# Kernel optimization log

Hardware: AMD Instinct MI355X
Metric: run time of the kernel (lower is better)

Reference implementation:

```python
import jax, jax.numpy as jnp
import numpy as np

E = 1024
H = 16
CH = E // H

def setup_inputs() -> dict:
    key = jax.random.key(0)
    ks = jax.random.split(key, 9)
    s = E ** -0.5
    return {
        'x': jax.random.normal(ks[0], (4, 2048, E), dtype=jnp.float32),
        'Wq': jax.random.normal(ks[1], (E, E), dtype=jnp.float32) * s,
        'bq': jnp.zeros((E,), dtype=jnp.float32),
        'Wk': jax.random.normal(ks[2], (E, E), dtype=jnp.float32) * s,
        'bk': jnp.zeros((E,), dtype=jnp.float32),
        'Wv': jax.random.normal(ks[3], (E, E), dtype=jnp.float32) * s,
        'bv': jnp.zeros((E,), dtype=jnp.float32),
        'Wo': jax.random.normal(ks[4], (E, E), dtype=jnp.float32) * s,
        'bo': jnp.zeros((E,), dtype=jnp.float32),
    }

def _split_heads(t):
    # [..., n, H*ch] -> [..., H, n, ch]
    b, n, e = t.shape
    return t.reshape(b, n, H, CH).transpose(0, 2, 1, 3)

def reference(x, Wq, bq, Wk, bk, Wv, bv, Wo, bo):
    scale = CH ** -0.5
    q = _split_heads(x @ Wq.T + bq)  # [b,H,n,ch]
    k = _split_heads(x @ Wk.T + bk)
    v = _split_heads(x @ Wv.T + bv)
    att = jnp.einsum('bhqc,bhkc->bhqk', q, k) * scale
    att = jax.nn.softmax(att, axis=-1)
    out = jnp.einsum('bhqk,bhkc->bhqc', att, v)  # [b,H,n,ch]
    b, h, n, c = out.shape
    out = out.transpose(0, 2, 1, 3).reshape(b, n, h * c)
    return out @ Wo.T + bo
```

## Files before the change

### kernel.cpp

```cpp
#include <hip/hip_runtime.h>
#include <stdint.h>

#define EMB   1024
#define NHEAD 16
#define CHD   64
#define NB    4
#define SEQ   2048
#define NTOK  (NB * SEQ)
#define KDIM  1024

typedef __attribute__((ext_vector_type(8))) short  bf16x8;
typedef __attribute__((ext_vector_type(4))) short  short4v;
typedef __attribute__((ext_vector_type(4))) float  f32x4;
typedef __attribute__((ext_vector_type(4))) float  float4v;

__device__ __forceinline__ short f2bf(float f) {
    unsigned int u = __float_as_uint(f);
    u += 0x7fffu + ((u >> 16) & 1u);
    return (short)(u >> 16);
}

__device__ __forceinline__ void async16(const short* g, short* l) {
    __builtin_amdgcn_global_load_lds((__attribute__((address_space(1))) void const*)g,
                                     (__attribute__((address_space(3))) void*)l, 16, 0, 0);
}

__global__ __launch_bounds__(256) void cvt_all(const float* __restrict__ x,
                                               const float* __restrict__ Wq,
                                               const float* __restrict__ Wk,
                                               const float* __restrict__ Wv,
                                               const float* __restrict__ Wo,
                                               short* __restrict__ xb,
                                               short* __restrict__ Wqb,
                                               short* __restrict__ Wkb,
                                               short* __restrict__ Wvb,
                                               short* __restrict__ Wob) {
    int bid = blockIdx.x;
    const float* src;
    short* dst;
    int idx;
    if (bid < 8192) {
        src = x; dst = xb; idx = bid * 256 + threadIdx.x;
    } else {
        int w  = (bid - 8192) >> 10;
        int lb = (bid - 8192) & 1023;
        src = (w == 0) ? Wq : (w == 1) ? Wk : (w == 2) ? Wv : Wo;
        dst = (w == 0) ? Wqb : (w == 1) ? Wkb : (w == 2) ? Wvb : Wob;
        idx = lb * 256 + threadIdx.x;
    }
    float4v v = ((const float4v*)src)[idx];
    short4v s;
    s.x = f2bf(v.x); s.y = f2bf(v.y); s.z = f2bf(v.z); s.w = f2bf(v.w);
    ((short4v*)dst)[idx] = s;
}

__device__ __forceinline__ void gemm_core(const short* __restrict__ Atile,
                                          const short* __restrict__ Btile,
                                          short* As, short* Bs, f32x4 acc[4][4]) {
    const int tid  = threadIdx.x;
    const int wave = tid >> 6, lane = tid & 63;
    const int quad = lane >> 4, l16 = lane & 15;
    const int wm = (wave >> 1) * 64, wn = (wave & 1) * 64;
    const int srow = lane >> 2;
    const int scol = (lane & 3) * 8;

    for (int k0 = 0; k0 < KDIM; k0 += 32) {
        __syncthreads();
#pragma unroll
        for (int c = 0; c < 2; ++c) {
            int chunk = wave * 2 + c;
            int row = chunk * 16 + srow;
            async16(Atile + (size_t)row * KDIM + k0 + scol, As + chunk * 512);
            async16(Btile + (size_t)row * KDIM + k0 + scol, Bs + chunk * 512);
        }
        __syncthreads();
        bf16x8 af[4], bfr[4];
#pragma unroll
        for (int i = 0; i < 4; ++i)
            af[i] = *(const bf16x8*)&As[(wm + i * 16 + l16) * 32 + quad * 8];
#pragma unroll
        for (int j = 0; j < 4; ++j)
            bfr[j] = *(const bf16x8*)&Bs[(wn + j * 16 + l16) * 32 + quad * 8];
#pragma unroll
        for (int i = 0; i < 4; ++i)
#pragma unroll
            for (int j = 0; j < 4; ++j)
                acc[i][j] = __builtin_amdgcn_mfma_f32_16x16x32_bf16(af[i], bfr[j], acc[i][j], 0, 0, 0);
    }
}

#define QSCALE 0.1803368801111204f


#define MFMA16(A,B,C) __builtin_amdgcn_mfma_f32_16x16x32_bf16(A,B,C,0,0,0)
#define BARR  { __builtin_amdgcn_s_barrier(); __builtin_amdgcn_sched_barrier(0); }
#define VMC4  asm volatile("s_waitcnt vmcnt(4)" ::: "memory");
#define VMC0  asm volatile("s_waitcnt vmcnt(0)" ::: "memory");
#define PRIO1 __builtin_amdgcn_s_setprio(1);
#define PRIO0 __builtin_amdgcn_s_setprio(0);

#define STAGE_A_(BUF,H,T) { \
    async16(aS0 + (size_t)(H)*131072 + (T)*64, sm + (BUF)*32768 + (H)*8192 + stA); \
    async16(aS1 + (size_t)(H)*131072 + (T)*64, sm + (BUF)*32768 + (H)*8192 + 4096 + stA); }
#define STAGE_B_(BUF,H,T) { \
    async16(bS0 + (size_t)(H)*131072 + (T)*64, sm + (BUF)*32768 + 16384 + (H)*8192 + stA); \
    async16(bS1 + (size_t)(H)*131072 + (T)*64, sm + (BUF)*32768 + 16384 + (H)*8192 + 4096 + stA); }

#define LDB_(BUF) { \
    const short* _pb = sm + (BUF)*32768 + bro; \
    bfr[0][0] = *(const bf16x8*)(_pb + ac0);        bfr[0][1] = *(const bf16x8*)(_pb + ac1); \
    bfr[1][0] = *(const bf16x8*)(_pb + 1024 + ac0); bfr[1][1] = *(const bf16x8*)(_pb + 1024 + ac1); \
    bfr[2][0] = *(const bf16x8*)(_pb + 2048 + ac0); bfr[2][1] = *(const bf16x8*)(_pb + 2048 + ac1); \
    bfr[3][0] = *(const bf16x8*)(_pb + 3072 + ac0); bfr[3][1] = *(const bf16x8*)(_pb + 3072 + ac1); }

#define LDA_(BUF,Q) { \
    const short* _pa = sm + (BUF)*32768 + aro + (Q)*2048; \
    af[0][0] = *(const bf16x8*)(_pa + ac0);        af[0][1] = *(const bf16x8*)(_pa + ac1); \
    af[1][0] = *(const bf16x8*)(_pa + 1024 + ac0); af[1][1] = *(const bf16x8*)(_pa + 1024 + ac1); }

#define MF_(Q) { \
    acc[2*(Q)][0]   = MFMA16(af[0][0], bfr[0][0], acc[2*(Q)][0]); \
    acc[2*(Q)][0]   = MFMA16(af[0][1], bfr[0][1], acc[2*(Q)][0]); \
    acc[2*(Q)][1]   = MFMA16(af[0][0], bfr[1][0], acc[2*(Q)][1]); \
    acc[2*(Q)][1]   = MFMA16(af[0][1], bfr[1][1], acc[2*(Q)][1]); \
    acc[2*(Q)][2]   = MFMA16(af[0][0], bfr[2][0], acc[2*(Q)][2]); \
    acc[2*(Q)][2]   = MFMA16(af[0][1], bfr[2][1], acc[2*(Q)][2]); \
    acc[2*(Q)][3]   = MFMA16(af[0][0], bfr[3][0], acc[2*(Q)][3]); \
    acc[2*(Q)][3]   = MFMA16(af[0][1], bfr[3][1], acc[2*(Q)][3]); \
    acc[2*(Q)+1][0] = MFMA16(af[1][0], bfr[0][0], acc[2*(Q)+1][0]); \
    acc[2*(Q)+1][0] = MFMA16(af[1][1], bfr[0][1], acc[2*(Q)+1][0]); \
    acc[2*(Q)+1][1] = MFMA16(af[1][0], bfr[1][0], acc[2*(Q)+1][1]); \
    acc[2*(Q)+1][1] = MFMA16(af[1][1], bfr[1][1], acc[2*(Q)+1][1]); \
    acc[2*(Q)+1][2] = MFMA16(af[1][0], bfr[2][0], acc[2*(Q)+1][2]); \
    acc[2*(Q)+1][2] = MFMA16(af[1][1], bfr[2][1], acc[2*(Q)+1][2]); \
    acc[2*(Q)+1][3] = MFMA16(af[1][0], bfr[3][0], acc[2*(Q)+1][3]); \
    acc[2*(Q)+1][3] = MFMA16(af[1][1], bfr[3][1], acc[2*(Q)+1][3]); }

#define WINDOW(RB, AB, TA, BB, TB) \
    LDB_(RB) LDA_(RB,0) STAGE_A_(AB,0,TA) BARR \
    PRIO1 MF_(0) PRIO0 BARR \
    LDA_(RB,1) STAGE_A_(AB,1,TA) BARR \
    PRIO1 MF_(1) PRIO0 BARR \
    LDA_(RB,2) STAGE_B_(BB,0,TB) BARR \
    PRIO1 MF_(2) PRIO0 BARR \
    LDA_(RB,3) STAGE_B_(BB,1,TB) BARR \
    PRIO1 MF_(3) PRIO0 VMC4 BARR

__global__ __launch_bounds__(512, 2) void qk256(const short* __restrict__ xb,
                                                const short* __restrict__ Wqk,
                                                const float* __restrict__ bq,
                                                const float* __restrict__ bk,
                                                short* __restrict__ Qb,
                                                short* __restrict__ Kb) {
    extern __shared__ short sm[];
    const int bm = blockIdx.x, bn = blockIdx.y;
    const int tid = threadIdx.x;
    const int w = tid >> 6, lane = tid & 63;
    const int kq = lane >> 4, l16 = lane & 15;
    const int wmi = w >> 2, wni = w & 3;

    const int colsw = ((lane & 7) * 8) ^ (((lane >> 5) & 1) << 4);
    const short* aS0 = xb  + (size_t)(bm * 256 + w * 8 + (lane >> 3)) * 1024 + colsw;
    const short* aS1 = aS0 + (size_t)64 * 1024;
    const short* bS0 = Wqk + (size_t)(bn * 256 + w * 8 + (lane >> 3)) * 1024 + colsw;
    const short* bS1 = bS0 + (size_t)64 * 1024;
    const int stA = w * 512;

    const int swz = (l16 & 4) ? 16 : 0;
    const int ac0 = (kq * 8) ^ swz;
    const int ac1 = (32 + kq * 8) ^ swz;
    const int aro = wmi * 8192 + l16 * 64;
    const int bro = 16384 + (wni >> 1) * 8192 + ((wni & 1) * 64 + l16) * 64;

    f32x4 acc[8][4];
    const f32x4 z = {0.f, 0.f, 0.f, 0.f};
#pragma unroll
    for (int m = 0; m < 8; ++m)
#pragma unroll
        for (int n = 0; n < 4; ++n) acc[m][n] = z;
    bf16x8 bfr[4][2], af[2][2];

    STAGE_A_(0,0,0) STAGE_A_(0,1,0) STAGE_B_(0,0,0) STAGE_B_(0,1,0)
    STAGE_B_(1,0,1) STAGE_B_(1,1,1)
    VMC4 BARR

    for (int it = 0; it < 7; ++it) {
        const int te = 2 * it;
        WINDOW(0, 1, te + 1, 0, te + 2)
        WINDOW(1, 0, te + 2, 1, te + 3)
    }
    LDB_(0) LDA_(0,0) STAGE_A_(1,0,15) BARR
    PRIO1 MF_(0) PRIO0 BARR
    LDA_(0,1) STAGE_A_(1,1,15) BARR
    PRIO1 MF_(1) PRIO0 BARR
    LDA_(0,2) BARR
    PRIO1 MF_(2) PRIO0 BARR
    LDA_(0,3) BARR
    PRIO1 MF_(3) PRIO0 VMC0 BARR
    LDB_(1)
    LDA_(1,0) MF_(0)
    LDA_(1,1) MF_(1)
    LDA_(1,2) MF_(2)
    LDA_(1,3) MF_(3)

    const bool isQ = (bn < 4);
    const float* bias = isQ ? bq : bk;
    short* dst = isQ ? Qb : Kb;
    const float sc = isQ ? QSCALE : 1.0f;
    const int fb = (bn & 3) * 256 + wni * 64 + l16;
    const int tok0 = bm * 256 + wmi * 128 + kq * 4;
#pragma unroll
    for (int n = 0; n < 4; ++n) {
        const int e = fb + n * 16;
        const int hh = e >> 6, cc = e & 63;
        const float bv_ = bias[e];
#pragma unroll
        for (int m = 0; m < 8; ++m)
#pragma unroll
            for (int r = 0; r < 4; ++r) {
                const int tok = tok0 + m * 16 + r;
                const int bb = tok >> 11, nn = tok & 2047;
                dst[(((size_t)bb * NHEAD + hh) * SEQ + nn) * CHD + cc] =
                    f2bf((acc[m][n][r] + bv_) * sc);
            }
    }
}

__global__ __launch_bounds__(256) void vproj(const short* __restrict__ xb,
                                             const short* __restrict__ Wvb,
                                             const float* __restrict__ bv,
                                             short* __restrict__ Vtb) {
    __shared__ short As[128 * 32], Bs[128 * 32];
    const int bm = blockIdx.x;
    const int ew = blockIdx.y * 128;

    f32x4 acc[4][4];
    const f32x4 z = {0.f, 0.f, 0.f, 0.f};
#pragma unroll
    for (int i = 0; i < 4; ++i)
#pragma unroll
        for (int j = 0; j < 4; ++j) acc[i][j] = z;

    gemm_core(Wvb + (size_t)ew * KDIM, xb + (size_t)bm * 128 * KDIM, As, Bs, acc);

    const int lane = threadIdx.x & 63, wave = threadIdx.x >> 6;
    const int quad = lane >> 4, l16 = lane & 15;
    const int wm = (wave >> 1) * 64, wn = (wave & 1) * 64;
#pragma unroll
    for (int i = 0; i < 4; ++i)
#pragma unroll
        for (int j = 0; j < 4; ++j)
#pragma unroll
            for (int r = 0; r < 4; ++r) {
                int e = ew + wm + i * 16 + quad * 4 + r;
                int token = bm * 128 + wn + j * 16 + l16;
                int bb = token >> 11, nn = token & 2047;
                int hh = e >> 6, cc = e & 63;
                Vtb[(((size_t)bb * NHEAD + hh) * CHD + cc) * SEQ + nn] =
                    f2bf(acc[i][j][r] + bv[e]);
            }
}

__global__ __launch_bounds__(256, 4) void attn(const short* __restrict__ Qb,
                                               const short* __restrict__ Kb,
                                               const short* __restrict__ Vtb,
                                               short* __restrict__ AOb) {
    __shared__ short Ks[16 * 512];
    __shared__ short Vs[16 * 512];

    const int lid = blockIdx.x;
    const int bh = (lid & 7) * 8 + (lid >> 7);
    const int qt = (lid >> 3) & 15;

    const int tid = threadIdx.x, wave = tid >> 6, lane = tid & 63;
    const int quad = lane >> 4, l16 = lane & 15;

    const short* Kg = Kb  + (size_t)bh * SEQ * CHD;
    const short* Vg = Vtb + (size_t)bh * CHD * SEQ;

    bf16x8 qf0[2], qf1[2];
#pragma unroll
    for (int g = 0; g < 2; ++g) {
        const short* Qg = Qb + ((size_t)bh * SEQ + qt * 128 + wave * 32 + g * 16 + l16) * CHD;
        qf0[g] = *(const bf16x8*)(Qg + quad * 8);
        qf1[g] = *(const bf16x8*)(Qg + 32 + quad * 8);
    }

    const int kr = lane >> 3, ku = (lane & 7) ^ kr;
    const int vr = lane >> 4, vu = (lane & 15) ^ (vr << 2);

    int koff[4], voff[4];
#pragma unroll
    for (int cc = 0; cc < 4; ++cc) {
        int c = wave * 4 + cc;
        int l = c * 8 + kr;
        int j = l >> 4, m = l & 15;
        int kvg = ((j >> 1) << 5) + ((m >> 2) << 3) + ((j & 1) << 2) + (m & 3);
        koff[cc] = kvg * CHD + ku * 8;
        voff[cc] = (c * 4 + vr) * SEQ + vu * 8;
    }

    const int krow = l16 & 7;
    const int kbase = ((l16 >> 3) * 512) + krow * 64;
    const short* kp0 = Ks + kbase + ((quad ^ krow) << 3);
    const short* kp1 = Ks + kbase + (((4 + quad) ^ krow) << 3);
    const int vrow = l16 & 3;
    const short* vp = Vs + (l16 >> 2) * 512 + vrow * 128 + quad * 8;

    const f32x4 zf = {0.f, 0.f, 0.f, 0.f};
    const bf16x8 onesv = {16256, 16256, 16256, 16256, 16256, 16256, 16256, 16256};
    f32x4 O[2][4];
#pragma unroll
    for (int g = 0; g < 2; ++g)
#pragma unroll
        for (int nb = 0; nb < 4; ++nb) O[g][nb] = zf;
    f32x4 lacc[2];
    lacc[0] = zf; lacc[1] = zf;

#define ATTN_STAGE_K(T) { \
    const short* _kg = Kg + (size_t)(T) * (128 * CHD); \
    _Pragma("unroll") \
    for (int cc = 0; cc < 4; ++cc) \
        async16(_kg + koff[cc], Ks + (wave * 4 + cc) * 512); }
#define ATTN_STAGE_V(T) { \
    const short* _vg = Vg + (size_t)(T) * 128; \
    _Pragma("unroll") \
    for (int cc = 0; cc < 4; ++cc) \
        async16(_vg + voff[cc], Vs + (wave * 4 + cc) * 512); }

#define ATTN_SPHASE { \
    _Pragma("unroll") \
    for (int kk = 0; kk < 4; ++kk) { \
        bf16x8 kA0 = *(const bf16x8*)(kp0 + (2 * kk) * 1024); \
        bf16x8 kA1 = *(const bf16x8*)(kp1 + (2 * kk) * 1024); \
        bf16x8 kB0 = *(const bf16x8*)(kp0 + (2 * kk + 1) * 1024); \
        bf16x8 kB1 = *(const bf16x8*)(kp1 + (2 * kk + 1) * 1024); \
        _Pragma("unroll") \
        for (int g = 0; g < 2; ++g) { \
            PRIO1 \
            f32x4 sA = MFMA16(kA0, qf0[g], zf); \
            sA = MFMA16(kA1, qf1[g], sA); \
            f32x4 sB = MFMA16(kB0, qf0[g], zf); \
            sB = MFMA16(kB1, qf1[g], sB); \
            PRIO0 \
            unsigned a0 = __float_as_uint(__builtin_amdgcn_exp2f(sA.x)); \
            unsigned a1 = __float_as_uint(__builtin_amdgcn_exp2f(sA.y)); \
            unsigned a2 = __float_as_uint(__builtin_amdgcn_exp2f(sA.z)); \
            unsigned a3 = __float_as_uint(__builtin_amdgcn_exp2f(sA.w)); \
            unsigned b0 = __float_as_uint(__builtin_amdgcn_exp2f(sB.x)); \
            unsigned b1 = __float_as_uint(__builtin_amdgcn_exp2f(sB.y)); \
            unsigned b2 = __float_as_uint(__builtin_amdgcn_exp2f(sB.z)); \
            unsigned b3 = __float_as_uint(__builtin_amdgcn_exp2f(sB.w)); \
            pf[kk][g].i[0] = __builtin_amdgcn_perm(a1, a0, 0x07060302u); \
            pf[kk][g].i[1] = __builtin_amdgcn_perm(a3, a2, 0x07060302u); \
            pf[kk][g].i[2] = __builtin_amdgcn_perm(b1, b0, 0x07060302u); \
            pf[kk][g].i[3] = __builtin_amdgcn_perm(b3, b2, 0x07060302u); \
            lacc[g] = MFMA16(pf[kk][g].v, onesv, lacc[g]); \
        } \
    } }

#define ATTN_PVPHASE { \
    _Pragma("unroll") \
    for (int kk = 0; kk < 4; ++kk) { \
        const short* vpk = vp + ((kk ^ vrow) << 5); \
        PRIO1 \
        _Pragma("unroll") \
        for (int nb = 0; nb < 4; ++nb) { \
            bf16x8 vf = *(const bf16x8*)(vpk + nb * 2048); \
            _Pragma("unroll") \
            for (int g = 0; g < 2; ++g) \
                O[g][nb] = MFMA16(pf[kk][g].v, vf, O[g][nb]); \
        } \
        PRIO0 \
    } }

    ATTN_STAGE_K(0) ATTN_STAGE_V(0)
    VMC4 BARR

    for (int kt = 0; kt < 15; ++kt) {
        union { int i[4]; bf16x8 v; } pf[4][2];
        ATTN_SPHASE
        BARR
        ATTN_STAGE_K(kt + 1)
        VMC4
        BARR
        ATTN_PVPHASE
        BARR
        ATTN_STAGE_V(kt + 1)
        VMC4
        BARR
    }
    {
        union { int i[4]; bf16x8 v; } pf[4][2];
        ATTN_SPHASE
        VMC0 BARR
        ATTN_PVPHASE
    }

    const int b = bh >> 4, h = bh & 15;
#pragma unroll
    for (int g = 0; g < 2; ++g) {
        float linv[4];
#pragma unroll
        for (int r = 0; r < 4; ++r) linv[r] = 1.0f / lacc[g][r];
#pragma unroll
        for (int nb = 0; nb < 4; ++nb)
#pragma unroll
            for (int r = 0; r < 4; ++r) {
                int n = qt * 128 + wave * 32 + g * 16 + quad * 4 + r;
                int cc = nb * 16 + l16;
                AOb[((size_t)b * SEQ + n) * EMB + h * CHD + cc] = f2bf(O[g][nb][r] * linv[r]);
            }
    }
#undef ATTN_STAGE_K
#undef ATTN_STAGE_V
#undef ATTN_SPHASE
#undef ATTN_PVPHASE
}

__global__ __launch_bounds__(256) void out_gemm(const short* __restrict__ AOb,
                                                const short* __restrict__ Wob,
                                                const float* __restrict__ bo,
                                                float* __restrict__ out) {
    __shared__ short As[128 * 32], Bs[128 * 32];
    const int bm = blockIdx.x, bn = blockIdx.y;

    f32x4 acc[4][4];
    const f32x4 z = {0.f, 0.f, 0.f, 0.f};
#pragma unroll
    for (int i = 0; i < 4; ++i)
#pragma unroll
        for (int j = 0; j < 4; ++j) acc[i][j] = z;

    gemm_core(AOb + (size_t)bm * 128 * KDIM, Wob + (size_t)bn * 128 * KDIM, As, Bs, acc);

    const int lane = threadIdx.x & 63, wave = threadIdx.x >> 6;
    const int quad = lane >> 4, l16 = lane & 15;
    const int wm = (wave >> 1) * 64, wn = (wave & 1) * 64;
#pragma unroll
    for (int i = 0; i < 4; ++i)
#pragma unroll
        for (int j = 0; j < 4; ++j)
#pragma unroll
            for (int r = 0; r < 4; ++r) {
                int token = bm * 128 + wm + i * 16 + quad * 4 + r;
                int e = bn * 128 + wn + j * 16 + l16;
                out[(size_t)token * EMB + e] = acc[i][j][r] + bo[e];
            }
}

extern "C" void kernel_launch(void* const* d_in, const int* in_sizes, int n_in,
                              void* d_out, int out_size, void* d_ws, size_t ws_size,
                              hipStream_t stream) {
    const float* x  = (const float*)d_in[0];
    const float* Wq = (const float*)d_in[1];
    const float* bq = (const float*)d_in[2];
    const float* Wk = (const float*)d_in[3];
    const float* bk = (const float*)d_in[4];
    const float* Wv = (const float*)d_in[5];
    const float* bv = (const float*)d_in[6];
    const float* Wo = (const float*)d_in[7];
    const float* bo = (const float*)d_in[8];

    char* ws = (char*)d_ws;
    short* xb  = (short*)(ws + 0);
    short* Wqb = (short*)(ws + (size_t)16 * 1024 * 1024);
    short* Wkb = (short*)(ws + (size_t)18 * 1024 * 1024);
    short* Wvb = (short*)(ws + (size_t)20 * 1024 * 1024);
    short* Wob = (short*)(ws + (size_t)22 * 1024 * 1024);
    short* Qb  = (short*)(ws + (size_t)24 * 1024 * 1024);
    short* Kb  = (short*)(ws + (size_t)40 * 1024 * 1024);
    short* Vtb = (short*)(ws + (size_t)56 * 1024 * 1024);
    short* AOb = (short*)(ws + (size_t)72 * 1024 * 1024);

    static bool s_cfg = false;
    if (!s_cfg) {
        hipFuncSetAttribute(reinterpret_cast<const void*>(qk256),
                            hipFuncAttributeMaxDynamicSharedMemorySize, 131072);
        s_cfg = true;
    }

    cvt_all<<<dim3(8192 + 4096), dim3(256), 0, stream>>>(x, Wq, Wk, Wv, Wo,
                                                         xb, Wqb, Wkb, Wvb, Wob);
    qk256<<<dim3(32, 8), dim3(512), 131072, stream>>>(xb, Wqb, bq, bk, Qb, Kb);
    vproj<<<dim3(64, 8), dim3(256), 0, stream>>>(xb, Wvb, bv, Vtb);
    attn<<<dim3(1024), dim3(256), 0, stream>>>(Qb, Kb, Vtb, AOb);
    out_gemm<<<dim3(64, 8), dim3(256), 0, stream>>>(AOb, Wob, bo, (float*)d_out);
}
```

Baseline: 275.0 us.

## Double-buffer K/V tiles in attention and fuse score and PV phases per chunk

The attention kernel now keeps two shared-memory buffers for K and V, prefetching tile t+2 while computing tile t, and interleaves score/exp and PV MFMAs per 32-key chunk instead of running them as separate phases. This removes the serialized stage-wait-barrier sequence between the S and PV phases and shrinks the live P registers. In exchange, LDS per block doubles and the occupancy hint drops from 4 to 2 blocks per CU, so latency hiding depends more on in-block overlap.

```diff
diff --git a/kernel.cpp b/kernel.cpp
--- a/kernel.cpp
+++ b/kernel.cpp
@@ -95,6 +95,7 @@
 #define MFMA16(A,B,C) __builtin_amdgcn_mfma_f32_16x16x32_bf16(A,B,C,0,0,0)
 #define BARR  { __builtin_amdgcn_s_barrier(); __builtin_amdgcn_sched_barrier(0); }
 #define VMC4  asm volatile("s_waitcnt vmcnt(4)" ::: "memory");
+#define VMC8  asm volatile("s_waitcnt vmcnt(8)" ::: "memory");
 #define VMC0  asm volatile("s_waitcnt vmcnt(0)" ::: "memory");
 #define PRIO1 __builtin_amdgcn_s_setprio(1);
 #define PRIO0 __builtin_amdgcn_s_setprio(0);
@@ -261,12 +262,12 @@
             }
 }
 
-__global__ __launch_bounds__(256, 4) void attn(const short* __restrict__ Qb,
+__global__ __launch_bounds__(256, 2) void attn(const short* __restrict__ Qb,
                                                const short* __restrict__ Kb,
                                                const short* __restrict__ Vtb,
                                                short* __restrict__ AOb) {
-    __shared__ short Ks[16 * 512];
-    __shared__ short Vs[16 * 512];
+    __shared__ short Ks[2][8192];
+    __shared__ short Vs[2][8192];
 
     const int lid = blockIdx.x;
     const int bh = (lid & 7) * 8 + (lid >> 7);
@@ -299,13 +300,15 @@
         koff[cc] = kvg * CHD + ku * 8;
         voff[cc] = (c * 4 + vr) * SEQ + vu * 8;
     }
+    short* ksBase = &Ks[0][0];
+    short* vsBase = &Vs[0][0];
 
     const int krow = l16 & 7;
     const int kbase = ((l16 >> 3) * 512) + krow * 64;
-    const short* kp0 = Ks + kbase + ((quad ^ krow) << 3);
-    const short* kp1 = Ks + kbase + (((4 + quad) ^ krow) << 3);
+    const short* kp0 = ksBase + kbase + ((quad ^ krow) << 3);
+    const short* kp1 = ksBase + kbase + (((4 + quad) ^ krow) << 3);
     const int vrow = l16 & 3;
-    const short* vp = Vs + (l16 >> 2) * 512 + vrow * 128 + quad * 8;
+    const short* vp = vsBase + (l16 >> 2) * 512 + vrow * 128 + quad * 8;
 
     const f32x4 zf = {0.f, 0.f, 0.f, 0.f};
     const bf16x8 onesv = {16256, 16256, 16256, 16256, 16256, 16256, 16256, 16256};
@@ -317,24 +320,26 @@
     f32x4 lacc[2];
     lacc[0] = zf; lacc[1] = zf;
 
-#define ATTN_STAGE_K(T) { \
+#define ATTN_STAGE(BUF, T) { \
     const short* _kg = Kg + (size_t)(T) * (128 * CHD); \
-    _Pragma("unroll") \
-    for (int cc = 0; cc < 4; ++cc) \
-        async16(_kg + koff[cc], Ks + (wave * 4 + cc) * 512); }
-#define ATTN_STAGE_V(T) { \
     const short* _vg = Vg + (size_t)(T) * 128; \
     _Pragma("unroll") \
-    for (int cc = 0; cc < 4; ++cc) \
-        async16(_vg + voff[cc], Vs + (wave * 4 + cc) * 512); }
-
-#define ATTN_SPHASE { \
+    for (int cc = 0; cc < 4; ++cc) { \
+        async16(_kg + koff[cc], ksBase + (BUF) * 8192 + (wave * 4 + cc) * 512); \
+        async16(_vg + voff[cc], vsBase + (BUF) * 8192 + (wave * 4 + cc) * 512); \
+    } }
+
+#define ATTN_COMPUTE(BUF) { \
+    const short* kb0 = kp0 + (BUF) * 8192; \
+    const short* kb1 = kp1 + (BUF) * 8192; \
+    const short* vb  = vp  + (BUF) * 8192; \
     _Pragma("unroll") \
     for (int kk = 0; kk < 4; ++kk) { \
-        bf16x8 kA0 = *(const bf16x8*)(kp0 + (2 * kk) * 1024); \
-        bf16x8 kA1 = *(const bf16x8*)(kp1 + (2 * kk) * 1024); \
-        bf16x8 kB0 = *(const bf16x8*)(kp0 + (2 * kk + 1) * 1024); \
-        bf16x8 kB1 = *(const bf16x8*)(kp1 + (2 * kk + 1) * 1024); \
+        bf16x8 kA0 = *(const bf16x8*)(kb0 + (2 * kk) * 1024); \
+        bf16x8 kA1 = *(const bf16x8*)(kb1 + (2 * kk) * 1024); \
+        bf16x8 kB0 = *(const bf16x8*)(kb0 + (2 * kk + 1) * 1024); \
+        bf16x8 kB1 = *(const bf16x8*)(kb1 + (2 * kk + 1) * 1024); \
+        union { int i[4]; bf16x8 v; } pf[2]; \
         _Pragma("unroll") \
         for (int g = 0; g < 2; ++g) { \
             PRIO1 \
@@ -351,51 +356,44 @@
             unsigned b1 = __float_as_uint(__builtin_amdgcn_exp2f(sB.y)); \
             unsigned b2 = __float_as_uint(__builtin_amdgcn_exp2f(sB.z)); \
             unsigned b3 = __float_as_uint(__builtin_amdgcn_exp2f(sB.w)); \
-            pf[kk][g].i[0] = __builtin_amdgcn_perm(a1, a0, 0x07060302u); \
-            pf[kk][g].i[1] = __builtin_amdgcn_perm(a3, a2, 0x07060302u); \
-            pf[kk][g].i[2] = __builtin_amdgcn_perm(b1, b0, 0x07060302u); \
-            pf[kk][g].i[3] = __builtin_amdgcn_perm(b3, b2, 0x07060302u); \
-            lacc[g] = MFMA16(pf[kk][g].v, onesv, lacc[g]); \
+            pf[g].i[0] = __builtin_amdgcn_perm(a1, a0, 0x07060302u); \
+            pf[g].i[1] = __builtin_amdgcn_perm(a3, a2, 0x07060302u); \
+            pf[g].i[2] = __builtin_amdgcn_perm(b1, b0, 0x07060302u); \
+            pf[g].i[3] = __builtin_amdgcn_perm(b3, b2, 0x07060302u); \
+            lacc[g] = MFMA16(pf[g].v, onesv, lacc[g]); \
         } \
-    } }
-
-#define ATTN_PVPHASE { \
-    _Pragma("unroll") \
-    for (int kk = 0; kk < 4; ++kk) { \
-        const short* vpk = vp + ((kk ^ vrow) << 5); \
+        const short* vpk = vb + ((kk ^ vrow) << 5); \
         PRIO1 \
         _Pragma("unroll") \
         for (int nb = 0; nb < 4; ++nb) { \
             bf16x8 vf = *(const bf16x8*)(vpk + nb * 2048); \
             _Pragma("unroll") \
             for (int g = 0; g < 2; ++g) \
-                O[g][nb] = MFMA16(pf[kk][g].v, vf, O[g][nb]); \
+                O[g][nb] = MFMA16(pf[g].v, vf, O[g][nb]); \
         } \
         PRIO0 \
     } }
 
-    ATTN_STAGE_K(0) ATTN_STAGE_V(0)
-    VMC4 BARR
-
-    for (int kt = 0; kt < 15; ++kt) {
-        union { int i[4]; bf16x8 v; } pf[4][2];
-        ATTN_SPHASE
+    ATTN_STAGE(0, 0)
+    ATTN_STAGE(1, 1)
+
+    for (int it = 0; it < 7; ++it) {
+        VMC8 BARR
+        ATTN_COMPUTE(0)
         BARR
-        ATTN_STAGE_K(kt + 1)
-        VMC4
+        ATTN_STAGE(0, 2 * it + 2)
+        VMC8 BARR
+        ATTN_COMPUTE(1)
         BARR
-        ATTN_PVPHASE
-        BARR
-        ATTN_STAGE_V(kt + 1)
-        VMC4
-        BARR
-    }
-    {
-        union { int i[4]; bf16x8 v; } pf[4][2];
-        ATTN_SPHASE
-        VMC0 BARR
-        ATTN_PVPHASE
-    }
+        ATTN_STAGE(1, 2 * it + 3)
+    }
+    VMC8 BARR
+    ATTN_COMPUTE(0)
+    VMC0 BARR
+    ATTN_COMPUTE(1)
+
+#undef ATTN_STAGE
+#undef ATTN_COMPUTE
 
     const int b = bh >> 4, h = bh & 15;
 #pragma unroll
@@ -412,10 +410,6 @@
                 AOb[((size_t)b * SEQ + n) * EMB + h * CHD + cc] = f2bf(O[g][nb][r] * linv[r]);
             }
     }
-#undef ATTN_STAGE_K
-#undef ATTN_STAGE_V
-#undef ATTN_SPHASE
-#undef ATTN_PVPHASE
 }
 
 __global__ __launch_bounds__(256) void out_gemm(const short* __restrict__ AOb,
```

New measurement: 265.5 us. -3.4%, faster.
